# Performance work log

Hardware: AMD Instinct MI355X
Metric: run time of the kernel (lower is better)

## Reference

```python
import jax, jax.numpy as jnp
import numpy as np

N_EMBD = 768
N_HEAD = 8
HEAD_DIM = N_EMBD // N_HEAD
EPS = 1e-5


def _layernorm(x, g, b):
    mu = jnp.mean(x, axis=-1, keepdims=True)
    var = jnp.mean(jnp.square(x - mu), axis=-1, keepdims=True)
    return (x - mu) * jax.lax.rsqrt(var + EPS) * g + b


def _new_gelu(x):
    c = jnp.sqrt(2.0 / jnp.pi).astype(x.dtype)
    return 0.5 * x * (1.0 + jnp.tanh(c * (x + 0.044715 * x * x * x)))


def setup_inputs() -> dict:
    key = jax.random.key(0)
    ks = jax.random.split(key, 10)
    B, T, C = 16, 1024, N_EMBD
    s = lambda fan_in: 1.0 / np.sqrt(fan_in)
    inp = {
        "x": jax.random.normal(ks[0], (B, T, C), dtype=jnp.float32),
        "ln1_g": jnp.ones((C,), jnp.float32),
        "ln1_b": jnp.zeros((C,), jnp.float32),
        "attn_w": jax.random.normal(ks[1], (C, 3 * C), jnp.float32) * s(C),
        "attn_b": jnp.zeros((3 * C,), jnp.float32),
        "proj_w": jax.random.normal(ks[2], (C, C), jnp.float32) * s(C),
        "proj_b": jnp.zeros((C,), jnp.float32),
        "ln2_g": jnp.ones((C,), jnp.float32),
        "ln2_b": jnp.zeros((C,), jnp.float32),
        "fc_w": jax.random.normal(ks[3], (C, 4 * C), jnp.float32) * s(C),
        "fc_b": jnp.zeros((4 * C,), jnp.float32),
        "fc2_w": jax.random.normal(ks[4], (4 * C, C), jnp.float32) * s(4 * C),
        "fc2_b": jnp.zeros((C,), jnp.float32),
    }
    return inp


def reference(x, ln1_g, ln1_b, attn_w, attn_b, proj_w, proj_b,
              ln2_g, ln2_b, fc_w, fc_b, fc2_w, fc2_b):
    B, T, C = x.shape
    H, D = N_HEAD, HEAD_DIM
    scale = 1.0 / np.sqrt(D)

    # --- attention branch ---
    h = _layernorm(x, ln1_g, ln1_b)
    qkv = h @ attn_w + attn_b                       # [B,T,3C]
    q, k, v = jnp.split(qkv, 3, axis=-1)
    q = q.reshape(B, T, H, D).transpose(0, 2, 1, 3)  # [B,H,T,D]
    k = k.reshape(B, T, H, D).transpose(0, 2, 1, 3)
    v = v.reshape(B, T, H, D).transpose(0, 2, 1, 3)
    att = jnp.einsum("bhqd,bhkd->bhqk", q, k) * scale
    causal = jnp.tril(jnp.ones((T, T), bool))
    att = jnp.where(causal, att, -jnp.inf)
    att = jax.nn.softmax(att, axis=-1)
    y = jnp.einsum("bhqk,bhkd->bhqd", att, v)        # [B,H,T,D]
    y = y.transpose(0, 2, 1, 3).reshape(B, T, C)
    y = y @ proj_w + proj_b
    x = x + y

    # --- MLP branch ---
    h2 = _layernorm(x, ln2_g, ln2_b)
    h2 = _new_gelu(h2 @ fc_w + fc_b)
    x = x + (h2 @ fc2_w + fc2_b)
    return x
```

## Files before the change

### kernel.cpp

```cpp
#include <hip/hip_runtime.h>


typedef __bf16 bf16;
typedef __bf16 bf16x8 __attribute__((ext_vector_type(8)));
typedef __bf16 bf16x4 __attribute__((ext_vector_type(4)));
typedef __bf16 bf16x2 __attribute__((ext_vector_type(2)));
typedef float f32x4 __attribute__((ext_vector_type(4)));

__device__ __forceinline__ void async_copy16(const void* g, void* l)
{
    __builtin_amdgcn_global_load_lds((__attribute__((address_space(1))) void*)g,
                                     (__attribute__((address_space(3))) void*)l,
                                     16, 0, 0);
}

__global__ __launch_bounds__(256) void wtrans(const float* __restrict__ in,
                                              bf16* __restrict__ out,
                                              const int R, const int C)
{
    __shared__ float tile[32][33];
    const int c0 = blockIdx.x * 32, r0 = blockIdx.y * 32;
    const int tx = threadIdx.x, ty = threadIdx.y;
#pragma unroll
    for (int i = 0; i < 4; ++i)
        tile[ty + i * 8][tx] = in[(size_t)(r0 + ty + i * 8) * C + c0 + tx];
    __syncthreads();
#pragma unroll
    for (int i = 0; i < 4; ++i)
        out[(size_t)(c0 + ty + i * 8) * R + r0 + tx] = (bf16)tile[tx][ty + i * 8];
}

template <typename TIN>
__global__ __launch_bounds__(256) void ln_kernel(const TIN* __restrict__ x,
                                                 const float* __restrict__ g,
                                                 const float* __restrict__ bb,
                                                 bf16* __restrict__ out)
{
    const int wave = threadIdx.x >> 6, lane = threadIdx.x & 63;
    const size_t row = (size_t)blockIdx.x * 4 + wave;
    const TIN* xr = x + row * 768;
    float v[12];
    float s = 0.f;
#pragma unroll
    for (int c = 0; c < 3; ++c) {
        if constexpr (sizeof(TIN) == 2) {
            const bf16x4 t4 = *(const bf16x4*)(xr + c * 256 + lane * 4);
#pragma unroll
            for (int j = 0; j < 4; ++j) { v[c * 4 + j] = (float)t4[j]; s += v[c * 4 + j]; }
        } else {
            const float4 t4 = *(const float4*)(xr + c * 256 + lane * 4);
            v[c * 4 + 0] = t4.x; v[c * 4 + 1] = t4.y;
            v[c * 4 + 2] = t4.z; v[c * 4 + 3] = t4.w;
            s += t4.x + t4.y + t4.z + t4.w;
        }
    }
#pragma unroll
    for (int off = 32; off >= 1; off >>= 1) s += __shfl_xor(s, off, 64);
    const float mu = s * (1.f / 768.f);
    float q = 0.f;
#pragma unroll
    for (int i = 0; i < 12; ++i) { const float d = v[i] - mu; q += d * d; }
#pragma unroll
    for (int off = 32; off >= 1; off >>= 1) q += __shfl_xor(q, off, 64);
    const float rs = rsqrtf(q * (1.f / 768.f) + 1e-5f);
#pragma unroll
    for (int c = 0; c < 3; ++c) {
        const float4 gv = *(const float4*)(g + c * 256 + lane * 4);
        const float4 bv = *(const float4*)(bb + c * 256 + lane * 4);
        bf16x4 ov;
        ov[0] = (bf16)((v[c * 4 + 0] - mu) * rs * gv.x + bv.x);
        ov[1] = (bf16)((v[c * 4 + 1] - mu) * rs * gv.y + bv.y);
        ov[2] = (bf16)((v[c * 4 + 2] - mu) * rs * gv.z + bv.z);
        ov[3] = (bf16)((v[c * 4 + 3] - mu) * rs * gv.w + bv.w);
        *(bf16x4*)(out + row * 768 + c * 256 + lane * 4) = ov;
    }
}

template <int EPI, int TN>
__global__ __launch_bounds__(256) void gemm_bt(const bf16* __restrict__ A,
                                               const bf16* __restrict__ Bt,
                                               const float* __restrict__ bias,
                                               const void* __restrict__ res,
                                               void* __restrict__ out,
                                               const int M, const int N, const int K)
{
    constexpr int NT_W = TN / 32;
    constexpr int NCPB = (TN * 8) / 256;
    __shared__ bf16 sA[2 * 128 * 32];
    __shared__ bf16 sB[2 * TN * 32];
    const int t = threadIdx.x;
    const int wave = t >> 6, lane = t & 63;
    const int quad = lane >> 4, l16 = lane & 15;
    const int bm0 = blockIdx.y * 128, bn0 = blockIdx.x * TN;
    const int wm = (wave >> 1) * 64, wn = (wave & 1) * (TN / 2);

    const f32x4 z4 = {0.f, 0.f, 0.f, 0.f};
    f32x4 acc[4][NT_W];
#pragma unroll
    for (int i = 0; i < 4; ++i)
#pragma unroll
        for (int j = 0; j < NT_W; ++j) acc[i][j] = z4;

    const bf16* gAp[4]; bf16* lAp[4];
#pragma unroll
    for (int c = 0; c < 4; ++c) {
        const int j = c * 256 + t;
        const int img = j >> 9, r = (j >> 2) & 127, k8 = j & 3;
        gAp[c] = A + (size_t)(bm0 + r) * K + img * 32 + k8 * 8;
        lAp[c] = sA + j * 8;
    }
    const bf16* gBp[NCPB]; bf16* lBp[NCPB];
#pragma unroll
    for (int c = 0; c < NCPB; ++c) {
        const int j = c * 256 + t;
        const int img = j / (TN * 4), r = (j % (TN * 4)) >> 2, k8 = j & 3;
        gBp[c] = Bt + (size_t)(bn0 + r) * K + img * 32 + k8 * 8;
        lBp[c] = sB + j * 8;
    }

    for (int kt = 0; kt < K; kt += 64) {
        __syncthreads();
#pragma unroll
        for (int c = 0; c < 4; ++c) async_copy16(gAp[c] + kt, lAp[c]);
#pragma unroll
        for (int c = 0; c < NCPB; ++c) async_copy16(gBp[c] + kt, lBp[c]);
        __syncthreads();

#pragma unroll
        for (int ks = 0; ks < 2; ++ks) {
            bf16x8 af[4], bfm[NT_W];
#pragma unroll
            for (int mt = 0; mt < 4; ++mt)
                af[mt] = *(const bf16x8*)(sA + ks * 4096 +
                                          (wm + mt * 16 + l16) * 32 + quad * 8);
#pragma unroll
            for (int nt = 0; nt < NT_W; ++nt)
                bfm[nt] = *(const bf16x8*)(sB + ks * (TN * 32) +
                                           (wn + nt * 16 + l16) * 32 + quad * 8);
#pragma unroll
            for (int mt = 0; mt < 4; ++mt)
#pragma unroll
                for (int nt = 0; nt < NT_W; ++nt)
                    acc[mt][nt] = __builtin_amdgcn_mfma_f32_16x16x32_bf16(
                        af[mt], bfm[nt], acc[mt][nt], 0, 0, 0);
        }
    }

    const int rb = bm0 + wm + quad * 4;
    const int cb = bn0 + wn + l16;
#pragma unroll
    for (int mt = 0; mt < 4; ++mt) {
#pragma unroll
        for (int nt = 0; nt < NT_W; ++nt) {
            const int col = cb + nt * 16;
            const float bv = bias[col];
#pragma unroll
            for (int reg = 0; reg < 4; ++reg) {
                const size_t idx = (size_t)(rb + mt * 16 + reg) * N + col;
                float v = acc[mt][nt][reg] + bv;
                if constexpr (EPI == 1) {
                    ((bf16*)out)[idx] = (bf16)(v + ((const float*)res)[idx]);
                } else if constexpr (EPI == 2) {
                    const float u = v;
                    const float a2 = 1.5957691216057308f *
                                     (u + 0.044715f * u * u * u);
                    v = u / (1.f + __expf(-a2));
                    ((bf16*)out)[idx] = (bf16)v;
                } else if constexpr (EPI == 3) {
                    ((float*)out)[idx] = v + (float)((const bf16*)res)[idx];
                } else {
                    ((bf16*)out)[idx] = (bf16)v;
                }
            }
        }
    }
}

__global__ __launch_bounds__(256) void attn_kernel(const bf16* __restrict__ qkv,
                                                   bf16* __restrict__ aout)
{
    constexpr int T = 1024, C3 = 2304, HD = 96, CC = 768;
    __shared__ bf16 sK[64 * 104];
    __shared__ bf16 sV[96 * 72];
    __shared__ bf16 sP[4][16 * 76];
    const int tid = threadIdx.x;
    const int wave = tid >> 6, lane = tid & 63;
    const int quad = lane >> 4, l16 = lane & 15;
    const int bh = blockIdx.x, b = bh >> 3, h = bh & 7;
    const float scale = 0.10206207261596575f;

    const int qAi = blockIdx.y;
    const int qBi = 15 - qAi;
    const int q0A = qAi * 64 + wave * 16;
    const int q0B = qBi * 64 + wave * 16;

    const bf16* kgbase = qkv + (size_t)b * T * C3 + CC + h * HD;
    const bf16* vgbase = qkv + (size_t)b * T * C3 + 2 * CC + h * HD;
    bf16* sPw = &sP[wave][0];

    int kKey[3], kCh[3], vKey2[3], vDq[3];
#pragma unroll
    for (int c = 0; c < 3; ++c) {
        const int j = c * 256 + tid;
        kKey[c] = j / 12; kCh[c] = j - kKey[c] * 12;
        vKey2[c] = (j & 31) * 2; vDq[c] = j >> 5;
    }

    const bf16* qrA = qkv + (size_t)(b * T + q0A + l16) * C3 + h * HD + quad * 8;
    const bf16* qrB = qkv + (size_t)(b * T + q0B + l16) * C3 + h * HD + quad * 8;
    const bf16x8 aQA0 = *(const bf16x8*)(qrA);
    const bf16x8 aQA1 = *(const bf16x8*)(qrA + 32);
    const bf16x8 aQA2 = *(const bf16x8*)(qrA + 64);
    const bf16x8 aQB0 = *(const bf16x8*)(qrB);
    const bf16x8 aQB1 = *(const bf16x8*)(qrB + 32);
    const bf16x8 aQB2 = *(const bf16x8*)(qrB + 64);

    const f32x4 z4 = {0.f, 0.f, 0.f, 0.f};
    f32x4 oA[6], oB[6];
#pragma unroll
    for (int i = 0; i < 6; ++i) { oA[i] = z4; oB[i] = z4; }
    float lA[4] = {0.f, 0.f, 0.f, 0.f}, lB[4] = {0.f, 0.f, 0.f, 0.f};

    auto process = [&](const bf16x8& Q0, const bf16x8& Q1, const bf16x8& Q2,
                       f32x4 (&o)[6], float (&lrow)[4],
                       const int q0, const int kk0, const bool diag) {
        f32x4 s[4];
#pragma unroll
        for (int i = 0; i < 4; ++i) s[i] = z4;
#pragma unroll
        for (int nt = 0; nt < 4; ++nt) {
            const bf16* kp = sK + (nt * 16 + l16) * 104 + quad * 8;
            const bf16x8 b0 = *(const bf16x8*)(kp);
            const bf16x8 b1 = *(const bf16x8*)(kp + 32);
            const bf16x8 b2 = *(const bf16x8*)(kp + 64);
            s[nt] = __builtin_amdgcn_mfma_f32_16x16x32_bf16(Q0, b0, s[nt], 0, 0, 0);
            s[nt] = __builtin_amdgcn_mfma_f32_16x16x32_bf16(Q1, b1, s[nt], 0, 0, 0);
            s[nt] = __builtin_amdgcn_mfma_f32_16x16x32_bf16(Q2, b2, s[nt], 0, 0, 0);
        }

        float psum[4] = {0.f, 0.f, 0.f, 0.f};
#pragma unroll
        for (int nt = 0; nt < 4; ++nt)
#pragma unroll
            for (int reg = 0; reg < 4; ++reg) {
                float v = s[nt][reg] * scale;
                if (diag) {
                    const int qr = q0 + quad * 4 + reg;
                    const int key = kk0 + nt * 16 + l16;
                    v = (key > qr) ? -1e30f : v;
                }
                const float p = __expf(fminf(v, 30.f));
                s[nt][reg] = p;
                psum[reg] += p;
            }

#pragma unroll
        for (int nt = 0; nt < 4; ++nt)
#pragma unroll
            for (int reg = 0; reg < 4; ++reg)
                sPw[(quad * 4 + reg) * 76 + nt * 16 + l16] = (bf16)s[nt][reg];
        __asm__ volatile("s_waitcnt lgkmcnt(0)" ::: "memory");

#pragma unroll
        for (int off = 1; off < 16; off <<= 1)
#pragma unroll
            for (int reg = 0; reg < 4; ++reg)
                psum[reg] += __shfl_xor(psum[reg], off, 64);
#pragma unroll
        for (int reg = 0; reg < 4; ++reg) lrow[reg] += psum[reg];

        const bf16x8 aP0 = *(const bf16x8*)(sPw + l16 * 76 + quad * 8);
        const bf16x8 aP1 = *(const bf16x8*)(sPw + l16 * 76 + 32 + quad * 8);
#pragma unroll
        for (int dd = 0; dd < 6; ++dd) {
            const bf16* vp = sV + (dd * 16 + l16) * 72 + quad * 8;
            const bf16x8 v0 = *(const bf16x8*)(vp);
            const bf16x8 v1 = *(const bf16x8*)(vp + 32);
            o[dd] = __builtin_amdgcn_mfma_f32_16x16x32_bf16(aP0, v0, o[dd], 0, 0, 0);
            o[dd] = __builtin_amdgcn_mfma_f32_16x16x32_bf16(aP1, v1, o[dd], 0, 0, 0);
        }
    };

    for (int kb = 0; kb <= qBi; ++kb) {
        const int kk0 = kb * 64;

        __syncthreads();
#pragma unroll
        for (int c = 0; c < 3; ++c) {
            const bf16x8 kv = *(const bf16x8*)(kgbase +
                                (size_t)(kk0 + kKey[c]) * C3 + kCh[c] * 8);
            *(bf16x8*)(sK + kKey[c] * 104 + kCh[c] * 8) = kv;
        }
#pragma unroll
        for (int c = 0; c < 3; ++c) {
            const bf16* p0 = vgbase + (size_t)(kk0 + vKey2[c]) * C3 + vDq[c] * 4;
            const bf16x4 va = *(const bf16x4*)p0;
            const bf16x4 vb = *(const bf16x4*)(p0 + C3);
#pragma unroll
            for (int jj = 0; jj < 4; ++jj) {
                bf16x2 pk; pk[0] = va[jj]; pk[1] = vb[jj];
                *(bf16x2*)(sV + (vDq[c] * 4 + jj) * 72 + vKey2[c]) = pk;
            }
        }
        __syncthreads();

        process(aQB0, aQB1, aQB2, oB, lB, q0B, kk0, kb == qBi);
        if (kb <= qAi)
            process(aQA0, aQA1, aQA2, oA, lA, q0A, kk0, kb == qAi);
    }

    bf16* opA = aout + (size_t)(b * T + q0A + quad * 4) * CC + h * HD + l16;
    bf16* opB = aout + (size_t)(b * T + q0B + quad * 4) * CC + h * HD + l16;
#pragma unroll
    for (int reg = 0; reg < 4; ++reg) {
        const float invA = 1.f / lA[reg];
        const float invB = 1.f / lB[reg];
#pragma unroll
        for (int dd = 0; dd < 6; ++dd) {
            opA[(size_t)reg * CC + dd * 16] = (bf16)(oA[dd][reg] * invA);
            opB[(size_t)reg * CC + dd * 16] = (bf16)(oB[dd][reg] * invB);
        }
    }
}

extern "C" void kernel_launch(void* const* d_in, const int* in_sizes, int n_in,
                              void* d_out, int out_size, void* d_ws, size_t ws_size,
                              hipStream_t stream)
{
    const float* x      = (const float*)d_in[0];
    const float* ln1_g  = (const float*)d_in[1];
    const float* ln1_b  = (const float*)d_in[2];
    const float* attn_w = (const float*)d_in[3];
    const float* attn_b = (const float*)d_in[4];
    const float* proj_w = (const float*)d_in[5];
    const float* proj_b = (const float*)d_in[6];
    const float* ln2_g  = (const float*)d_in[7];
    const float* ln2_b  = (const float*)d_in[8];
    const float* fc_w   = (const float*)d_in[9];
    const float* fc_b   = (const float*)d_in[10];
    const float* fc2_w  = (const float*)d_in[11];
    const float* fc2_b  = (const float*)d_in[12];

    char* ws = (char*)d_ws;
    bf16*  attn_wT = (bf16*)(ws + 0);
    bf16*  proj_wT = (bf16*)(ws + 3538944);
    bf16*  fc_wT   = (bf16*)(ws + 4718592);
    bf16*  fc2_wT  = (bf16*)(ws + 9437184);
    bf16*  hbuf    = (bf16*)(ws + 14155776);
    bf16*  qkv     = (bf16*)(ws + 39321600);
    bf16*  x1      = (bf16*)(ws + 39321600);
    bf16*  act     = (bf16*)(ws + 64487424);

    const dim3 tb(32, 8);

    wtrans<<<dim3(72, 24), tb, 0, stream>>>(attn_w, attn_wT, 768, 2304);
    wtrans<<<dim3(24, 24), tb, 0, stream>>>(proj_w, proj_wT, 768, 768);
    wtrans<<<dim3(96, 24), tb, 0, stream>>>(fc_w, fc_wT, 768, 3072);
    wtrans<<<dim3(24, 96), tb, 0, stream>>>(fc2_w, fc2_wT, 3072, 768);

    ln_kernel<float><<<4096, 256, 0, stream>>>(x, ln1_g, ln1_b, hbuf);

    gemm_bt<0, 128><<<dim3(18, 128), 256, 0, stream>>>(
        hbuf, attn_wT, attn_b, nullptr, qkv, 16384, 2304, 768);

    attn_kernel<<<dim3(128, 8), 256, 0, stream>>>(qkv, hbuf);

    gemm_bt<1, 128><<<dim3(6, 128), 256, 0, stream>>>(
        hbuf, proj_wT, proj_b, x, x1, 16384, 768, 768);

    ln_kernel<bf16><<<4096, 256, 0, stream>>>(x1, ln2_g, ln2_b, hbuf);

    for (int c = 0; c < 2; ++c) {
        const size_t ro = (size_t)c * 8192;
        gemm_bt<2, 128><<<dim3(24, 64), 256, 0, stream>>>(
            hbuf + ro * 768, fc_wT, fc_b, nullptr, act, 8192, 3072, 768);
        gemm_bt<3, 64><<<dim3(12, 64), 256, 0, stream>>>(
            act, fc2_wT, fc2_b, x1 + ro * 768,
            (float*)d_out + ro * 768, 8192, 768, 3072);
    }
}
```

Measured before the change: 663.8 us.

## Async-load K tiles into swizzled LDS and compute softmax row sums via MFMA

The K tile is now staged with global_load_lds direct-to-LDS copies into a 128-element-stride layout with an XOR swizzle, replacing register round-trip loads. The per-row softmax denominator is computed with an extra MFMA against a vector of ones instead of cross-lane shuffle reductions. The V tile row stride also changes from 72 to 68. The swizzled copy fetches 16 chunks per row where only 12 are used, so it moves extra bytes, and it relies on the barrier ordering the async LDS writes correctly.

```diff
diff --git a/kernel.cpp b/kernel.cpp
--- a/kernel.cpp
+++ b/kernel.cpp
@@ -180,8 +180,8 @@
                                                    bf16* __restrict__ aout)
 {
     constexpr int T = 1024, C3 = 2304, HD = 96, CC = 768;
-    __shared__ bf16 sK[64 * 104];
-    __shared__ bf16 sV[96 * 72];
+    __shared__ bf16 sK[64 * 128];
+    __shared__ bf16 sV[96 * 68];
     __shared__ bf16 sP[4][16 * 76];
     const int tid = threadIdx.x;
     const int wave = tid >> 6, lane = tid & 63;
@@ -198,11 +198,19 @@
     const bf16* vgbase = qkv + (size_t)b * T * C3 + 2 * CC + h * HD;
     bf16* sPw = &sP[wave][0];
 
-    int kKey[3], kCh[3], vKey2[3], vDq[3];
+    int kSrc[4]; bf16* kLds[4];
+#pragma unroll
+    for (int c = 0; c < 4; ++c) {
+        const int chunk = c * 256 + tid;
+        const int row = chunk >> 4, pos = chunk & 15;
+        const int dc = pos ^ (row & 7);
+        kSrc[c] = row * C3 + dc * 8;
+        kLds[c] = sK + chunk * 8;
+    }
+    int vKey2[3], vDq[3];
 #pragma unroll
     for (int c = 0; c < 3; ++c) {
         const int j = c * 256 + tid;
-        kKey[c] = j / 12; kCh[c] = j - kKey[c] * 12;
         vKey2[c] = (j & 31) * 2; vDq[c] = j >> 5;
     }
 
@@ -215,30 +223,35 @@
     const bf16x8 aQB1 = *(const bf16x8*)(qrB + 32);
     const bf16x8 aQB2 = *(const bf16x8*)(qrB + 64);
 
+    bf16x8 ones;
+#pragma unroll
+    for (int j = 0; j < 8; ++j) ones[j] = (bf16)1.0f;
+
     const f32x4 z4 = {0.f, 0.f, 0.f, 0.f};
     f32x4 oA[6], oB[6];
 #pragma unroll
     for (int i = 0; i < 6; ++i) { oA[i] = z4; oB[i] = z4; }
-    float lA[4] = {0.f, 0.f, 0.f, 0.f}, lB[4] = {0.f, 0.f, 0.f, 0.f};
+    f32x4 o7A = z4, o7B = z4;
 
     auto process = [&](const bf16x8& Q0, const bf16x8& Q1, const bf16x8& Q2,
-                       f32x4 (&o)[6], float (&lrow)[4],
+                       f32x4 (&o)[6], f32x4& o7,
                        const int q0, const int kk0, const bool diag) {
         f32x4 s[4];
 #pragma unroll
         for (int i = 0; i < 4; ++i) s[i] = z4;
 #pragma unroll
         for (int nt = 0; nt < 4; ++nt) {
-            const bf16* kp = sK + (nt * 16 + l16) * 104 + quad * 8;
-            const bf16x8 b0 = *(const bf16x8*)(kp);
-            const bf16x8 b1 = *(const bf16x8*)(kp + 32);
-            const bf16x8 b2 = *(const bf16x8*)(kp + 64);
+            const int rr = nt * 16 + l16;
+            const bf16* kpr = sK + rr * 128;
+            const int rx = rr & 7;
+            const bf16x8 b0 = *(const bf16x8*)(kpr + ((quad + 0) ^ rx) * 8);
+            const bf16x8 b1 = *(const bf16x8*)(kpr + ((quad + 4) ^ rx) * 8);
+            const bf16x8 b2 = *(const bf16x8*)(kpr + ((quad + 8) ^ rx) * 8);
             s[nt] = __builtin_amdgcn_mfma_f32_16x16x32_bf16(Q0, b0, s[nt], 0, 0, 0);
             s[nt] = __builtin_amdgcn_mfma_f32_16x16x32_bf16(Q1, b1, s[nt], 0, 0, 0);
             s[nt] = __builtin_amdgcn_mfma_f32_16x16x32_bf16(Q2, b2, s[nt], 0, 0, 0);
         }
 
-        float psum[4] = {0.f, 0.f, 0.f, 0.f};
 #pragma unroll
         for (int nt = 0; nt < 4; ++nt)
 #pragma unroll
@@ -249,9 +262,7 @@
                     const int key = kk0 + nt * 16 + l16;
                     v = (key > qr) ? -1e30f : v;
                 }
-                const float p = __expf(fminf(v, 30.f));
-                s[nt][reg] = p;
-                psum[reg] += p;
+                s[nt][reg] = __expf(fminf(v, 30.f));
             }
 
 #pragma unroll
@@ -261,19 +272,13 @@
                 sPw[(quad * 4 + reg) * 76 + nt * 16 + l16] = (bf16)s[nt][reg];
         __asm__ volatile("s_waitcnt lgkmcnt(0)" ::: "memory");
 
-#pragma unroll
-        for (int off = 1; off < 16; off <<= 1)
-#pragma unroll
-            for (int reg = 0; reg < 4; ++reg)
-                psum[reg] += __shfl_xor(psum[reg], off, 64);
-#pragma unroll
-        for (int reg = 0; reg < 4; ++reg) lrow[reg] += psum[reg];
-
         const bf16x8 aP0 = *(const bf16x8*)(sPw + l16 * 76 + quad * 8);
         const bf16x8 aP1 = *(const bf16x8*)(sPw + l16 * 76 + 32 + quad * 8);
+        o7 = __builtin_amdgcn_mfma_f32_16x16x32_bf16(aP0, ones, o7, 0, 0, 0);
+        o7 = __builtin_amdgcn_mfma_f32_16x16x32_bf16(aP1, ones, o7, 0, 0, 0);
 #pragma unroll
         for (int dd = 0; dd < 6; ++dd) {
-            const bf16* vp = sV + (dd * 16 + l16) * 72 + quad * 8;
+            const bf16* vp = sV + (dd * 16 + l16) * 68 + quad * 8;
             const bf16x8 v0 = *(const bf16x8*)(vp);
             const bf16x8 v1 = *(const bf16x8*)(vp + 32);
             o[dd] = __builtin_amdgcn_mfma_f32_16x16x32_bf16(aP0, v0, o[dd], 0, 0, 0);
@@ -286,11 +291,8 @@
 
         __syncthreads();
 #pragma unroll
-        for (int c = 0; c < 3; ++c) {
-            const bf16x8 kv = *(const bf16x8*)(kgbase +
-                                (size_t)(kk0 + kKey[c]) * C3 + kCh[c] * 8);
-            *(bf16x8*)(sK + kKey[c] * 104 + kCh[c] * 8) = kv;
-        }
+        for (int c = 0; c < 4; ++c)
+            async_copy16(kgbase + (size_t)kk0 * C3 + kSrc[c], kLds[c]);
 #pragma unroll
         for (int c = 0; c < 3; ++c) {
             const bf16* p0 = vgbase + (size_t)(kk0 + vKey2[c]) * C3 + vDq[c] * 4;
@@ -299,22 +301,22 @@
 #pragma unroll
             for (int jj = 0; jj < 4; ++jj) {
                 bf16x2 pk; pk[0] = va[jj]; pk[1] = vb[jj];
-                *(bf16x2*)(sV + (vDq[c] * 4 + jj) * 72 + vKey2[c]) = pk;
+                *(bf16x2*)(sV + (vDq[c] * 4 + jj) * 68 + vKey2[c]) = pk;
             }
         }
         __syncthreads();
 
-        process(aQB0, aQB1, aQB2, oB, lB, q0B, kk0, kb == qBi);
+        process(aQB0, aQB1, aQB2, oB, o7B, q0B, kk0, kb == qBi);
         if (kb <= qAi)
-            process(aQA0, aQA1, aQA2, oA, lA, q0A, kk0, kb == qAi);
+            process(aQA0, aQA1, aQA2, oA, o7A, q0A, kk0, kb == qAi);
     }
 
     bf16* opA = aout + (size_t)(b * T + q0A + quad * 4) * CC + h * HD + l16;
     bf16* opB = aout + (size_t)(b * T + q0B + quad * 4) * CC + h * HD + l16;
 #pragma unroll
     for (int reg = 0; reg < 4; ++reg) {
-        const float invA = 1.f / lA[reg];
-        const float invB = 1.f / lB[reg];
+        const float invA = 1.f / o7A[reg];
+        const float invB = 1.f / o7B[reg];
 #pragma unroll
         for (int dd = 0; dd < 6; ++dd) {
             opA[(size_t)reg * CC + dd * 16] = (bf16)(oA[dd][reg] * invA);
```

Measured after the change: 726.1 us. 9.4% more time.
